# Kernel tuning notes

Measured on AMD Instinct MI355X. Metric: run time of the kernel, lower is better.

## Reference

```python
import jax, jax.numpy as jnp
import numpy as np

M, K, N = 8192, 4096, 4096  # tokens, in_features, out_features


def setup_inputs() -> dict:
    key = jax.random.key(0)
    k1, k2, k3, k4 = jax.random.split(key, 4)
    inp = jax.random.normal(k1, (M, K), dtype=jnp.float32)
    # int8-range weights stored as int32 host-side; [out_features, in_features] like torch Linear
    weight = jax.random.randint(k2, (N, K), -128, 128, dtype=jnp.int32)
    weight_scale = jax.random.uniform(k3, (N,), dtype=jnp.float32, minval=1e-3, maxval=2e-2)
    bias = jax.random.normal(k4, (N,), dtype=jnp.float32)
    return {"input": inp, "weight": weight, "weight_scale": weight_scale, "bias": bias}


def reference(input, weight, weight_scale, bias):
    # --- init-time transforms (W8A8IntLinear.__init__) ---
    wq = weight.T.astype(jnp.int8)                                   # [K, N]
    azp_adj = jnp.sum(wq.astype(jnp.int32), axis=0, keepdims=True)    # [1, N] int32 column sums

    # --- dynamic asymmetric per-token int8 quantization (scaled_int8_quant) ---
    x_max = jnp.max(input, axis=-1, keepdims=True)                    # [M, 1]
    x_min = jnp.min(input, axis=-1, keepdims=True)                    # [M, 1]
    scale = (x_max - x_min) / 255.0                                   # per-token scale
    azp = jnp.round(-128.0 - x_min / scale).astype(jnp.int32)         # per-token zero point
    q = jnp.clip(jnp.round(input / scale).astype(jnp.int32) + azp, -128, 127).astype(jnp.int8)

    # --- int8 GEMM with int32 accumulation (cutlass_scaled_mm_azp) ---
    acc = jnp.matmul(q, wq, preferred_element_type=jnp.int32)         # [M, N] int32
    corrected = (acc - azp * azp_adj).astype(jnp.float32)             # zero-point correction
    return scale * weight_scale[None, :] * corrected + bias[None, :]
```

## Files before the change

### kernel.cpp

```cpp
#include <hip/hip_runtime.h>
#include <cstdint>
#include <cstddef>


#define M_DIM 8192
#define K_DIM 4096
#define N_DIM 4096
#define NT (K_DIM / 64)

typedef int v4i __attribute__((ext_vector_type(4)));

__global__ __launch_bounds__(256) void prep_kernel(
    const float* __restrict__ x, signed char* __restrict__ q,
    float* __restrict__ scale_out, int* __restrict__ azp_out,
    const int* __restrict__ w, signed char* __restrict__ w8,
    int* __restrict__ azp_adj)
{
    const int t = threadIdx.x;
    if (blockIdx.x < M_DIM) {
        const int m = blockIdx.x;
        const float4* row4 = (const float4*)(x + (size_t)m * K_DIM);

        float4 v[4];
        float mx = -3.4e38f, mn = 3.4e38f;
#pragma unroll
        for (int i = 0; i < 4; ++i) {
            v[i] = row4[i * 256 + t];
            mx = fmaxf(mx, fmaxf(fmaxf(v[i].x, v[i].y), fmaxf(v[i].z, v[i].w)));
            mn = fminf(mn, fminf(fminf(v[i].x, v[i].y), fminf(v[i].z, v[i].w)));
        }
#pragma unroll
        for (int off = 32; off; off >>= 1) {
            mx = fmaxf(mx, __shfl_down(mx, off));
            mn = fminf(mn, __shfl_down(mn, off));
        }
        __shared__ float smx[4], smn[4];
        if ((t & 63) == 0) { smx[t >> 6] = mx; smn[t >> 6] = mn; }
        __syncthreads();
        mx = fmaxf(fmaxf(smx[0], smx[1]), fmaxf(smx[2], smx[3]));
        mn = fminf(fminf(smn[0], smn[1]), fminf(smn[2], smn[3]));

        const float scale = (mx - mn) / 255.0f;
        const int azp = (int)rintf(-128.0f - mn / scale);
        if (t == 0) { scale_out[m] = scale; azp_out[m] = azp; }

        int* qrow = (int*)(q + (size_t)m * K_DIM);
        const float* vf = (const float*)v;
#pragma unroll
        for (int i = 0; i < 4; ++i) {
            int b[4];
#pragma unroll
            for (int j = 0; j < 4; ++j) {
                int qv = (int)rintf(vf[4 * i + j] / scale) + azp;
                qv = qv < -128 ? -128 : (qv > 127 ? 127 : qv);
                b[j] = qv;
            }
            qrow[i * 256 + t] =
                (b[0] & 255) | ((b[1] & 255) << 8) | ((b[2] & 255) << 16) | ((b[3] & 255) << 24);
        }
    } else {
        const int n = blockIdx.x - M_DIM;
        const int4* row = (const int4*)(w + (size_t)n * K_DIM);
        int* w8row = (int*)(w8 + (size_t)n * K_DIM);
        int sum = 0;
#pragma unroll
        for (int i = 0; i < 4; ++i) {
            int4 a = row[i * 256 + t];
            sum += a.x + a.y + a.z + a.w;
            w8row[i * 256 + t] =
                (a.x & 255) | ((a.y & 255) << 8) | ((a.z & 255) << 16) | ((a.w & 255) << 24);
        }
#pragma unroll
        for (int off = 32; off; off >>= 1) sum += __shfl_down(sum, off);
        __shared__ int ssum[4];
        if ((t & 63) == 0) ssum[t >> 6] = sum;
        __syncthreads();
        if (t == 0) azp_adj[n] = ssum[0] + ssum[1] + ssum[2] + ssum[3];
    }
}

__device__ __forceinline__ void async_copy16(const signed char* g, signed char* l) {
    __builtin_amdgcn_global_load_lds(
        (const __attribute__((address_space(1))) void*)g,
        (__attribute__((address_space(3))) void*)l, 16, 0, 0);
}

__device__ __forceinline__ void tile_compute(
    const v4i* a4, const v4i* b4, int abase, int bbase, v4i (&acc)[8][4])
{
    v4i af[4], bf[4], ah[4];
#pragma unroll
    for (int i = 0; i < 4; ++i) af[i] = a4[abase + i * 64];
#pragma unroll
    for (int i = 0; i < 4; ++i) bf[i] = b4[bbase + i * 64];
#pragma unroll
    for (int i = 0; i < 4; ++i) ah[i] = a4[abase + 256 + i * 64];
    __builtin_amdgcn_s_setprio(1);
#pragma unroll
    for (int i = 0; i < 4; ++i)
#pragma unroll
        for (int j = 0; j < 4; ++j)
            acc[i][j] = __builtin_amdgcn_mfma_i32_16x16x64_i8(af[i], bf[j], acc[i][j], 0, 0, 0);
#pragma unroll
    for (int i = 0; i < 4; ++i)
#pragma unroll
        for (int j = 0; j < 4; ++j)
            acc[4 + i][j] = __builtin_amdgcn_mfma_i32_16x16x64_i8(ah[i], bf[j], acc[4 + i][j], 0, 0, 0);
    __builtin_amdgcn_s_setprio(0);
}

__global__ __launch_bounds__(512, 2) void gemm_kernel(
    const signed char* __restrict__ A,
    const signed char* __restrict__ B,
    const float* __restrict__ scale, const int* __restrict__ azp,
    const int* __restrict__ azp_adj, const float* __restrict__ wscale,
    const float* __restrict__ bias, float* __restrict__ out)
{
    __shared__ signed char sA[4][16384];
    __shared__ signed char sB[4][16384];

    const int t = threadIdx.x;
    const int lane = t & 63;
    const int wave = t >> 6;
    const int quad = lane >> 4;
    const int r16 = lane & 15;

    int bid = blockIdx.y * gridDim.x + blockIdx.x;
    bid = (bid & 7) * 64 + (bid >> 3);
    const int bn = (bid & 15) << 8;
    const int bm = (bid >> 4) << 8;

    const int wm = (wave >> 2) << 7;
    const int wn = (wave & 3) << 6;

    v4i acc[8][4];
#pragma unroll
    for (int i = 0; i < 8; ++i)
#pragma unroll
        for (int j = 0; j < 4; ++j) acc[i][j] = (v4i){0, 0, 0, 0};

    const int srow = t >> 2;
    const int scol = ((t & 3) ^ ((t >> 3) & 3)) << 4;
    const signed char* ag0 = A + (size_t)(bm + srow) * K_DIM + scol;
    const signed char* ag1 = A + (size_t)(bm + 128 + srow) * K_DIM + scol;
    const signed char* bg0 = B + (size_t)(bn + srow) * K_DIM + scol;
    const signed char* bg1 = B + (size_t)(bn + 128 + srow) * K_DIM + scol;

#define STAGE_A(kt) do { const int _b = (kt) & 3; const int _ko = (kt) << 6; \
    async_copy16(ag0 + _ko, &sA[_b][t * 16]); \
    async_copy16(ag1 + _ko, &sA[_b][8192 + t * 16]); } while (0)
#define STAGE_B(kt) do { const int _b = (kt) & 3; const int _ko = (kt) << 6; \
    async_copy16(bg0 + _ko, &sB[_b][t * 16]); \
    async_copy16(bg1 + _ko, &sB[_b][8192 + t * 16]); } while (0)

    const int swz = quad ^ ((r16 >> 1) & 3);
    const v4i* a4 = (const v4i*)&sA[0][0];
    const v4i* b4 = (const v4i*)&sB[0][0];
    const int aIdx = (wm + r16) * 4 + swz;
    const int bIdx = (wn + r16) * 4 + swz;

    STAGE_A(0); STAGE_B(0);
    STAGE_A(1); STAGE_B(1);
    STAGE_A(2); STAGE_B(2);
    asm volatile("s_waitcnt vmcnt(8)\n\ts_barrier" ::: "memory");

    for (int kt = 0; kt < NT - 3; ++kt) {
        STAGE_A(kt + 3);
        STAGE_B(kt + 3);
        const int bb = kt & 3;
        tile_compute(a4, b4, aIdx + bb * 1024, bIdx + bb * 1024, acc);
        asm volatile("s_waitcnt vmcnt(8) lgkmcnt(0)\n\ts_barrier" ::: "memory");
    }
    tile_compute(a4, b4, aIdx + ((NT - 3) & 3) * 1024, bIdx + ((NT - 3) & 3) * 1024, acc);
    asm volatile("s_waitcnt vmcnt(4) lgkmcnt(0)\n\ts_barrier" ::: "memory");
    tile_compute(a4, b4, aIdx + ((NT - 2) & 3) * 1024, bIdx + ((NT - 2) & 3) * 1024, acc);
    asm volatile("s_waitcnt vmcnt(0) lgkmcnt(0)\n\ts_barrier" ::: "memory");
    tile_compute(a4, b4, aIdx + ((NT - 1) & 3) * 1024, bIdx + ((NT - 1) & 3) * 1024, acc);

#undef STAGE_A
#undef STAGE_B

#pragma unroll
    for (int i = 0; i < 8; ++i) {
        const int mbase = bm + wm + i * 16 + quad * 4;
        float sm[4]; int am[4];
#pragma unroll
        for (int r = 0; r < 4; ++r) { sm[r] = scale[mbase + r]; am[r] = azp[mbase + r]; }
#pragma unroll
        for (int j = 0; j < 4; ++j) {
            const int n = bn + wn + j * 16 + r16;
            const float wsn = wscale[n];
            const int adjn = azp_adj[n];
            const float bn_ = bias[n];
#pragma unroll
            for (int r = 0; r < 4; ++r) {
                const int c = acc[i][j][r] - am[r] * adjn;
                out[(size_t)(mbase + r) * N_DIM + n] = sm[r] * wsn * (float)c + bn_;
            }
        }
    }
}

extern "C" void kernel_launch(void* const* d_in, const int* in_sizes, int n_in,
                              void* d_out, int out_size, void* d_ws, size_t ws_size,
                              hipStream_t stream) {
    const float* x      = (const float*)d_in[0];
    const int*   w      = (const int*)d_in[1];
    const float* wscale = (const float*)d_in[2];
    const float* bias   = (const float*)d_in[3];
    float* out = (float*)d_out;

    char* ws = (char*)d_ws;
    signed char* q8  = (signed char*)ws;
    signed char* w8  = (signed char*)(ws + 33554432);
    float* scl       = (float*)(ws + 50331648);
    int*   azp       = (int*)(ws + 50331648 + 32768);
    int*   adj       = (int*)(ws + 50331648 + 65536);

    prep_kernel<<<M_DIM + N_DIM, 256, 0, stream>>>(x, q8, scl, azp, w, w8, adj);
    dim3 grid(N_DIM / 256, M_DIM / 256);
    gemm_kernel<<<grid, 512, 0, stream>>>(q8, w8, scl, azp, adj, wscale, bias, out);
}
```

Measured before the change: 425.3 us.

## Software-pipeline LDS fragment loads across k-tiles with split barriers and manual unroll

Restructures the GEMM main loop so the A/B register fragments for the next k-tile are read from LDS during the second half of the current tile's MFMAs, with double-buffered register fragments and a 4-way unrolled templated tile body. Barriers and waitcnts are split around two MFMA halves, with sched_barrier added to keep the compiler from reordering. The goal is to hide LDS read latency behind matrix-core work. The cost is more registers, which may pressure occupancy at 2 blocks per CU, and more delicate synchronisation.

```diff
diff --git a/kernel.cpp b/kernel.cpp
--- a/kernel.cpp
+++ b/kernel.cpp
@@ -6,7 +6,7 @@
 #define M_DIM 8192
 #define K_DIM 4096
 #define N_DIM 4096
-#define NT (K_DIM / 64)
+#define NT 64
 
 typedef int v4i __attribute__((ext_vector_type(4)));
 
@@ -85,28 +85,67 @@
         (__attribute__((address_space(3))) void*)l, 16, 0, 0);
 }
 
-__device__ __forceinline__ void tile_compute(
-    const v4i* a4, const v4i* b4, int abase, int bbase, v4i (&acc)[8][4])
+template<int RO>
+__device__ __forceinline__ void mfma16(const v4i (&x)[4], const v4i (&y)[4], v4i (&acc)[8][4]) {
+#pragma unroll
+    for (int i = 0; i < 4; ++i)
+#pragma unroll
+        for (int j = 0; j < 4; ++j)
+            acc[RO + i][j] = __builtin_amdgcn_mfma_i32_16x16x64_i8(x[i], y[j], acc[RO + i][j], 0, 0, 0);
+}
+
+template<int CUR, bool STG, int VMN, bool RA>
+__device__ __forceinline__ void tile_body(
+    int kt, signed char (*sA)[16384], signed char (*sB)[16384],
+    const signed char* ag0, const signed char* ag1,
+    const signed char* bg0, const signed char* bg1,
+    int t, int aIdx, int bIdx,
+    v4i (&af)[4], v4i (&bf)[4],
+    v4i (&afn)[4], v4i (&bfn)[4],
+    v4i (&acc)[8][4])
 {
-    v4i af[4], bf[4], ah[4];
-#pragma unroll
-    for (int i = 0; i < 4; ++i) af[i] = a4[abase + i * 64];
-#pragma unroll
-    for (int i = 0; i < 4; ++i) bf[i] = b4[bbase + i * 64];
-#pragma unroll
-    for (int i = 0; i < 4; ++i) ah[i] = a4[abase + 256 + i * 64];
+    const v4i* a4 = (const v4i*)&sA[CUR][0];
+
+    if constexpr (STG) {
+        const int ko = (kt + 3) << 6;
+        signed char* dA = &sA[(CUR + 3) & 3][0];
+        signed char* dB = &sB[(CUR + 3) & 3][0];
+        async_copy16(ag0 + ko, dA + t * 16);
+        async_copy16(ag1 + ko, dA + 8192 + t * 16);
+        async_copy16(bg0 + ko, dB + t * 16);
+        async_copy16(bg1 + ko, dB + 8192 + t * 16);
+    }
+    v4i ah[4];
+#pragma unroll
+    for (int i = 0; i < 4; ++i) ah[i] = a4[aIdx + 256 + i * 64];
+    if constexpr (VMN == 8)      asm volatile("s_waitcnt vmcnt(8)" ::: "memory");
+    else if constexpr (VMN == 4) asm volatile("s_waitcnt vmcnt(4)" ::: "memory");
+    else if constexpr (VMN == 0) asm volatile("s_waitcnt vmcnt(0)" ::: "memory");
+    asm volatile("s_barrier" ::: "memory");
+    asm volatile("s_waitcnt lgkmcnt(4)" ::: "memory");
+    __builtin_amdgcn_sched_barrier(0);
     __builtin_amdgcn_s_setprio(1);
-#pragma unroll
-    for (int i = 0; i < 4; ++i)
-#pragma unroll
-        for (int j = 0; j < 4; ++j)
-            acc[i][j] = __builtin_amdgcn_mfma_i32_16x16x64_i8(af[i], bf[j], acc[i][j], 0, 0, 0);
-#pragma unroll
-    for (int i = 0; i < 4; ++i)
-#pragma unroll
-        for (int j = 0; j < 4; ++j)
-            acc[4 + i][j] = __builtin_amdgcn_mfma_i32_16x16x64_i8(ah[i], bf[j], acc[4 + i][j], 0, 0, 0);
+    mfma16<0>(af, bf, acc);
     __builtin_amdgcn_s_setprio(0);
+    asm volatile("s_barrier" ::: "memory");
+
+    if constexpr (RA) {
+        const v4i* a4n = (const v4i*)&sA[(CUR + 1) & 3][0];
+        const v4i* b4n = (const v4i*)&sB[(CUR + 1) & 3][0];
+#pragma unroll
+        for (int i = 0; i < 4; ++i) {
+            afn[i] = a4n[aIdx + i * 64];
+            bfn[i] = b4n[bIdx + i * 64];
+        }
+        asm volatile("s_waitcnt lgkmcnt(8)" ::: "memory");
+    } else {
+        asm volatile("s_waitcnt lgkmcnt(0)" ::: "memory");
+    }
+    __builtin_amdgcn_sched_barrier(0);
+    __builtin_amdgcn_s_setprio(1);
+    mfma16<4>(ah, bf, acc);
+    __builtin_amdgcn_s_setprio(0);
+    asm volatile("s_barrier" ::: "memory");
 }
 
 __global__ __launch_bounds__(512, 2) void gemm_kernel(
@@ -154,28 +193,36 @@
     async_copy16(bg1 + _ko, &sB[_b][8192 + t * 16]); } while (0)
 
     const int swz = quad ^ ((r16 >> 1) & 3);
-    const v4i* a4 = (const v4i*)&sA[0][0];
-    const v4i* b4 = (const v4i*)&sB[0][0];
     const int aIdx = (wm + r16) * 4 + swz;
     const int bIdx = (wn + r16) * 4 + swz;
 
     STAGE_A(0); STAGE_B(0);
     STAGE_A(1); STAGE_B(1);
     STAGE_A(2); STAGE_B(2);
-    asm volatile("s_waitcnt vmcnt(8)\n\ts_barrier" ::: "memory");
-
-    for (int kt = 0; kt < NT - 3; ++kt) {
-        STAGE_A(kt + 3);
-        STAGE_B(kt + 3);
-        const int bb = kt & 3;
-        tile_compute(a4, b4, aIdx + bb * 1024, bIdx + bb * 1024, acc);
-        asm volatile("s_waitcnt vmcnt(8) lgkmcnt(0)\n\ts_barrier" ::: "memory");
-    }
-    tile_compute(a4, b4, aIdx + ((NT - 3) & 3) * 1024, bIdx + ((NT - 3) & 3) * 1024, acc);
-    asm volatile("s_waitcnt vmcnt(4) lgkmcnt(0)\n\ts_barrier" ::: "memory");
-    tile_compute(a4, b4, aIdx + ((NT - 2) & 3) * 1024, bIdx + ((NT - 2) & 3) * 1024, acc);
-    asm volatile("s_waitcnt vmcnt(0) lgkmcnt(0)\n\ts_barrier" ::: "memory");
-    tile_compute(a4, b4, aIdx + ((NT - 1) & 3) * 1024, bIdx + ((NT - 1) & 3) * 1024, acc);
+    asm volatile("s_waitcnt vmcnt(8)" ::: "memory");
+    asm volatile("s_barrier" ::: "memory");
+
+    v4i afA[4], bfA[4], afB[4], bfB[4];
+    {
+        const v4i* a4 = (const v4i*)&sA[0][0];
+        const v4i* b4 = (const v4i*)&sB[0][0];
+#pragma unroll
+        for (int i = 0; i < 4; ++i) {
+            afA[i] = a4[aIdx + i * 64];
+            bfA[i] = b4[bIdx + i * 64];
+        }
+    }
+
+    for (int kt = 0; kt < NT - 4; kt += 4) {
+        tile_body<0, true, 8, true>(kt,     sA, sB, ag0, ag1, bg0, bg1, t, aIdx, bIdx, afA, bfA, afB, bfB, acc);
+        tile_body<1, true, 8, true>(kt + 1, sA, sB, ag0, ag1, bg0, bg1, t, aIdx, bIdx, afB, bfB, afA, bfA, acc);
+        tile_body<2, true, 8, true>(kt + 2, sA, sB, ag0, ag1, bg0, bg1, t, aIdx, bIdx, afA, bfA, afB, bfB, acc);
+        tile_body<3, true, 8, true>(kt + 3, sA, sB, ag0, ag1, bg0, bg1, t, aIdx, bIdx, afB, bfB, afA, bfA, acc);
+    }
+    tile_body<0, true,  8, true >(NT - 4, sA, sB, ag0, ag1, bg0, bg1, t, aIdx, bIdx, afA, bfA, afB, bfB, acc);
+    tile_body<1, false, 4, true >(NT - 3, sA, sB, ag0, ag1, bg0, bg1, t, aIdx, bIdx, afB, bfB, afA, bfA, acc);
+    tile_body<2, false, 0, true >(NT - 2, sA, sB, ag0, ag1, bg0, bg1, t, aIdx, bIdx, afA, bfA, afB, bfB, acc);
+    tile_body<3, false, -1, false>(NT - 1, sA, sB, ag0, ag1, bg0, bg1, t, aIdx, bIdx, afB, bfB, afA, bfA, acc);
 
 #undef STAGE_A
 #undef STAGE_B
```

Result: faster. 402.4 us (-5.4%).

## Replace LDS-staged GEMM pipeline with direct global-to-register fragment loads

Applied to the files above, without the earlier changes.

Removes the shared-memory staging (global_load_lds into a 4-deep LDS ring with barriers). Each wave now loads its MFMA fragments straight from global memory into registers, double-buffered by hand across pairs of k-tiles. The block-to-tile mapping is also reworked into a grouped raster meant to improve L2 reuse. The aim is to drop LDS traffic and barrier synchronisation. In exchange, waves no longer share loaded tiles through LDS, so global and L2 traffic grows roughly by the reuse factor, and each load is an uncoalesced 16-byte access per lane.

```diff
diff --git a/kernel.cpp b/kernel.cpp
--- a/kernel.cpp
+++ b/kernel.cpp
@@ -6,7 +6,7 @@
 #define M_DIM 8192
 #define K_DIM 4096
 #define N_DIM 4096
-#define NT (K_DIM / 64)
+#define NT 64
 
 typedef int v4i __attribute__((ext_vector_type(4)));
 
@@ -79,34 +79,17 @@
     }
 }
 
-__device__ __forceinline__ void async_copy16(const signed char* g, signed char* l) {
-    __builtin_amdgcn_global_load_lds(
-        (const __attribute__((address_space(1))) void*)g,
-        (__attribute__((address_space(3))) void*)l, 16, 0, 0);
-}
-
-__device__ __forceinline__ void tile_compute(
-    const v4i* a4, const v4i* b4, int abase, int bbase, v4i (&acc)[8][4])
-{
-    v4i af[4], bf[4], ah[4];
-#pragma unroll
-    for (int i = 0; i < 4; ++i) af[i] = a4[abase + i * 64];
-#pragma unroll
-    for (int i = 0; i < 4; ++i) bf[i] = b4[bbase + i * 64];
-#pragma unroll
-    for (int i = 0; i < 4; ++i) ah[i] = a4[abase + 256 + i * 64];
-    __builtin_amdgcn_s_setprio(1);
+template<int RO>
+__device__ __forceinline__ void mfma16(const v4i (&x)[4], const v4i (&y)[4], v4i (&acc)[8][4]) {
 #pragma unroll
     for (int i = 0; i < 4; ++i)
 #pragma unroll
         for (int j = 0; j < 4; ++j)
-            acc[i][j] = __builtin_amdgcn_mfma_i32_16x16x64_i8(af[i], bf[j], acc[i][j], 0, 0, 0);
-#pragma unroll
-    for (int i = 0; i < 4; ++i)
-#pragma unroll
-        for (int j = 0; j < 4; ++j)
-            acc[4 + i][j] = __builtin_amdgcn_mfma_i32_16x16x64_i8(ah[i], bf[j], acc[4 + i][j], 0, 0, 0);
-    __builtin_amdgcn_s_setprio(0);
+            acc[RO + i][j] = __builtin_amdgcn_mfma_i32_16x16x64_i8(x[i], y[j], acc[RO + i][j], 0, 0, 0);
+}
+
+__device__ __forceinline__ v4i ldg16(const signed char* p) {
+    return *(const v4i*)p;
 }
 
 __global__ __launch_bounds__(512, 2) void gemm_kernel(
@@ -116,76 +99,70 @@
     const int* __restrict__ azp_adj, const float* __restrict__ wscale,
     const float* __restrict__ bias, float* __restrict__ out)
 {
-    __shared__ signed char sA[4][16384];
-    __shared__ signed char sB[4][16384];
-
     const int t = threadIdx.x;
     const int lane = t & 63;
     const int wave = t >> 6;
     const int quad = lane >> 4;
     const int r16 = lane & 15;
 
-    int bid = blockIdx.y * gridDim.x + blockIdx.x;
-    bid = (bid & 7) * 64 + (bid >> 3);
-    const int bn = (bid & 15) << 8;
-    const int bm = (bid >> 4) << 8;
+    const int i = blockIdx.y * gridDim.x + blockIdx.x;
+    const int r = i & 7, s = (i >> 3) & 31, rnd = i >> 8;
+    const int bm = (16 * rnd + 4 * (r >> 1) + (s >> 3)) << 8;
+    const int bn = (8 * (r & 1) + (s & 7)) << 8;
 
     const int wm = (wave >> 2) << 7;
     const int wn = (wave & 3) << 6;
 
     v4i acc[8][4];
 #pragma unroll
-    for (int i = 0; i < 8; ++i)
-#pragma unroll
-        for (int j = 0; j < 4; ++j) acc[i][j] = (v4i){0, 0, 0, 0};
-
-    const int srow = t >> 2;
-    const int scol = ((t & 3) ^ ((t >> 3) & 3)) << 4;
-    const signed char* ag0 = A + (size_t)(bm + srow) * K_DIM + scol;
-    const signed char* ag1 = A + (size_t)(bm + 128 + srow) * K_DIM + scol;
-    const signed char* bg0 = B + (size_t)(bn + srow) * K_DIM + scol;
-    const signed char* bg1 = B + (size_t)(bn + 128 + srow) * K_DIM + scol;
-
-#define STAGE_A(kt) do { const int _b = (kt) & 3; const int _ko = (kt) << 6; \
-    async_copy16(ag0 + _ko, &sA[_b][t * 16]); \
-    async_copy16(ag1 + _ko, &sA[_b][8192 + t * 16]); } while (0)
-#define STAGE_B(kt) do { const int _b = (kt) & 3; const int _ko = (kt) << 6; \
-    async_copy16(bg0 + _ko, &sB[_b][t * 16]); \
-    async_copy16(bg1 + _ko, &sB[_b][8192 + t * 16]); } while (0)
-
-    const int swz = quad ^ ((r16 >> 1) & 3);
-    const v4i* a4 = (const v4i*)&sA[0][0];
-    const v4i* b4 = (const v4i*)&sB[0][0];
-    const int aIdx = (wm + r16) * 4 + swz;
-    const int bIdx = (wn + r16) * 4 + swz;
-
-    STAGE_A(0); STAGE_B(0);
-    STAGE_A(1); STAGE_B(1);
-    STAGE_A(2); STAGE_B(2);
-    asm volatile("s_waitcnt vmcnt(8)\n\ts_barrier" ::: "memory");
-
-    for (int kt = 0; kt < NT - 3; ++kt) {
-        STAGE_A(kt + 3);
-        STAGE_B(kt + 3);
-        const int bb = kt & 3;
-        tile_compute(a4, b4, aIdx + bb * 1024, bIdx + bb * 1024, acc);
-        asm volatile("s_waitcnt vmcnt(8) lgkmcnt(0)\n\ts_barrier" ::: "memory");
-    }
-    tile_compute(a4, b4, aIdx + ((NT - 3) & 3) * 1024, bIdx + ((NT - 3) & 3) * 1024, acc);
-    asm volatile("s_waitcnt vmcnt(4) lgkmcnt(0)\n\ts_barrier" ::: "memory");
-    tile_compute(a4, b4, aIdx + ((NT - 2) & 3) * 1024, bIdx + ((NT - 2) & 3) * 1024, acc);
-    asm volatile("s_waitcnt vmcnt(0) lgkmcnt(0)\n\ts_barrier" ::: "memory");
-    tile_compute(a4, b4, aIdx + ((NT - 1) & 3) * 1024, bIdx + ((NT - 1) & 3) * 1024, acc);
-
-#undef STAGE_A
-#undef STAGE_B
-
-#pragma unroll
-    for (int i = 0; i < 8; ++i) {
-        const int mbase = bm + wm + i * 16 + quad * 4;
+    for (int ii = 0; ii < 8; ++ii)
+#pragma unroll
+        for (int j = 0; j < 4; ++j) acc[ii][j] = (v4i){0, 0, 0, 0};
+
+    const signed char* aBase = A + (size_t)(bm + wm + r16) * K_DIM + quad * 16;
+    const signed char* bBase = B + (size_t)(bn + wn + r16) * K_DIM + quad * 16;
+
+    v4i afP[4], bfP[4], afQ[4], bfQ[4], ah[4];
+
+#pragma unroll
+    for (int f = 0; f < 4; ++f) {
+        afP[f] = ldg16(aBase + f * 65536);
+        bfP[f] = ldg16(bBase + f * 65536);
+    }
+
+    for (int kt = 0; kt < NT; kt += 2) {
+        const int k0 = kt << 6;
+#pragma unroll
+        for (int f = 0; f < 4; ++f)
+            ah[f] = ldg16(aBase + 262144 + f * 65536 + k0);
+#pragma unroll
+        for (int f = 0; f < 4; ++f) {
+            afQ[f] = ldg16(aBase + f * 65536 + k0 + 64);
+            bfQ[f] = ldg16(bBase + f * 65536 + k0 + 64);
+        }
+        mfma16<0>(afP, bfP, acc);
+        mfma16<4>(ah, bfP, acc);
+
+#pragma unroll
+        for (int f = 0; f < 4; ++f)
+            ah[f] = ldg16(aBase + 262144 + f * 65536 + k0 + 64);
+        if (kt + 2 < NT) {
+#pragma unroll
+            for (int f = 0; f < 4; ++f) {
+                afP[f] = ldg16(aBase + f * 65536 + k0 + 128);
+                bfP[f] = ldg16(bBase + f * 65536 + k0 + 128);
+            }
+        }
+        mfma16<0>(afQ, bfQ, acc);
+        mfma16<4>(ah, bfQ, acc);
+    }
+
+#pragma unroll
+    for (int ii = 0; ii < 8; ++ii) {
+        const int mbase = bm + wm + ii * 16 + quad * 4;
         float sm[4]; int am[4];
 #pragma unroll
-        for (int r = 0; r < 4; ++r) { sm[r] = scale[mbase + r]; am[r] = azp[mbase + r]; }
+        for (int rr = 0; rr < 4; ++rr) { sm[rr] = scale[mbase + rr]; am[rr] = azp[mbase + rr]; }
 #pragma unroll
         for (int j = 0; j < 4; ++j) {
             const int n = bn + wn + j * 16 + r16;
@@ -193,9 +170,9 @@
             const int adjn = azp_adj[n];
             const float bn_ = bias[n];
 #pragma unroll
-            for (int r = 0; r < 4; ++r) {
-                const int c = acc[i][j][r] - am[r] * adjn;
-                out[(size_t)(mbase + r) * N_DIM + n] = sm[r] * wsn * (float)c + bn_;
+            for (int rr = 0; rr < 4; ++rr) {
+                const int c = acc[ii][j][rr] - am[rr] * adjn;
+                out[(size_t)(mbase + rr) * N_DIM + n] = sm[rr] * wsn * (float)c + bn_;
             }
         }
     }
```

Result: slower. 615.5 us (+44.7%).
